# Optimization experiments

Measured on AMD Instinct MI355X. Metric: run time of the kernel, lower is better.

Reference implementation:

```python
import jax, jax.numpy as jnp
import numpy as np

B, QLEN, DIM = 16, 1, 4096
H, HKV, HD = 32, 8, 128  # n_heads, n_kv_heads, head_dim
PREFIX = 8192            # tokens already in the static KV cache


def setup_inputs() -> dict:
    key = jax.random.key(0)
    ks = jax.random.split(key, 7)
    s = 0.02
    return {
        "x": jax.random.normal(ks[0], (B, QLEN, DIM), jnp.float32),
        "cache_k": jax.random.normal(ks[1], (B, PREFIX, HKV, HD), jnp.float32),
        "cache_v": jax.random.normal(ks[2], (B, PREFIX, HKV, HD), jnp.float32),
        "wq": jax.random.normal(ks[3], (H * HD, DIM), jnp.float32) * s,
        "wk": jax.random.normal(ks[4], (HKV * HD, DIM), jnp.float32) * s,
        "wv": jax.random.normal(ks[5], (HKV * HD, DIM), jnp.float32) * s,
        "wo": jax.random.normal(ks[6], (DIM, H * HD), jnp.float32) * s,
    }


def reference(x, cache_k, cache_v, wq, wk, wv, wo):
    """Decode step of AttentionWithKVCache (static cache, GQA).

    Equivalent to: write new K/V at start_pos=PREFIX, attend q over
    cache[:, :PREFIX+QLEN], repeat_kv to expand kv heads, SDPA, out proj.
    """
    b, s, _ = x.shape
    q = (x @ wq.T).reshape(b, s, H, HD)        # [B,S,H,D]
    k_new = (x @ wk.T).reshape(b, s, HKV, HD)  # [B,S,Hkv,D]
    v_new = (x @ wv.T).reshape(b, s, HKV, HD)
    # cache write == concat of prefix with new tokens
    k = jnp.concatenate([cache_k, k_new], axis=1)  # [B,K,Hkv,D]
    v = jnp.concatenate([cache_v, v_new], axis=1)
    rep = H // HKV
    # repeat_kv: expand+reshape repeats each kv head `rep` times consecutively
    k = jnp.repeat(k, rep, axis=2)  # [B,K,H,D]
    v = jnp.repeat(v, rep, axis=2)
    scale = 1.0 / jnp.sqrt(jnp.asarray(HD, dtype=q.dtype))
    scores = jnp.einsum("bqhd,bkhd->bhqk", q, k) * scale
    attn = jax.nn.softmax(scores.astype(jnp.float32), axis=-1).astype(q.dtype)
    out = jnp.einsum("bhqk,bkhd->bqhd", attn, v).reshape(b, s, H * HD)
    return out @ wo.T  # [B,S,DIM]
```

## Files before the change

kernel.cpp:

```cpp
#include <hip/hip_runtime.h>
#include <hip/hip_bf16.h>
#include <cstdint>
#include <cstddef>

#define DIM 4096
#define NB 16
#define NH 32
#define NKV 8
#define HD 128
#define PREFIX 8192
#define KPB 256
#define KPW 64
#define NCH (PREFIX / KPB)
#define NPART NCH

#define WS_QKV 0
#define WS_ATT (WS_QKV + NB * 6144)
#define WS_ML  (WS_ATT + NB * DIM)
#define WS_OP  (WS_ML + NB * NCH * 32 * 2)

typedef float f4_t __attribute__((ext_vector_type(4)));
typedef float f2_t __attribute__((ext_vector_type(2)));
__device__ __forceinline__ float4 ntload4(const float* p) {
  f4_t v = __builtin_nontemporal_load((const f4_t*)p);
  return make_float4(v.x, v.y, v.z, v.w);
}
__device__ __forceinline__ float2 ntload2(const float* p) {
  f2_t v = __builtin_nontemporal_load((const f2_t*)p);
  return make_float2(v.x, v.y);
}

template <int NW>
__global__ __launch_bounds__(NW * 64) void gemv16(
    const float* __restrict__ W0, const float* __restrict__ W1,
    const float* __restrict__ W2, int b1, int b2,
    const float* __restrict__ X, float* __restrict__ Y,
    int y_stride, int scale_rows, float scale) {
  __shared__ float xs[NB][2048];
  const int tid = threadIdx.x;
  const int wave = tid >> 6, lane = tid & 63;
  const int row_base = blockIdx.x * (NW * 4) + wave * 4;

  const float* Wp;
  if (row_base < b1)       Wp = W0 + (size_t)row_base * DIM;
  else if (row_base < b2)  Wp = W1 + (size_t)(row_base - b1) * DIM;
  else                     Wp = W2 + (size_t)(row_base - b2) * DIM;

  float acc[4][NB];
#pragma unroll
  for (int r = 0; r < 4; ++r)
#pragma unroll
    for (int b = 0; b < NB; ++b) acc[r][b] = 0.0f;

  for (int k0 = 0; k0 < DIM; k0 += 2048) {
    __syncthreads();
#pragma unroll
    for (int i = 0; i < (8192 + NW * 64 - 1) / (NW * 64); ++i) {
      const int idx = tid + i * (NW * 64);
      if (idx < 8192) {
        const int b = idx >> 9, c = idx & 511;
        ((float4*)&xs[b][0])[c] =
            ((const float4*)(X + (size_t)b * DIM + k0))[c];
      }
    }
    __syncthreads();
#pragma unroll 4
    for (int ii = 0; ii < 8; ++ii) {
      const int d = ii * 256 + lane * 4;
      float4 w4[4];
#pragma unroll
      for (int r = 0; r < 4; ++r)
        w4[r] = ntload4(Wp + (size_t)r * DIM + k0 + d);
#pragma unroll
      for (int b = 0; b < NB; ++b) {
        float4 x4 = *(const float4*)&xs[b][d];
#pragma unroll
        for (int r = 0; r < 4; ++r)
          acc[r][b] += w4[r].x * x4.x + w4[r].y * x4.y +
                       w4[r].z * x4.z + w4[r].w * x4.w;
      }
    }
  }

#pragma unroll
  for (int r = 0; r < 4; ++r)
#pragma unroll
    for (int b = 0; b < NB; ++b) {
      float v = acc[r][b];
#pragma unroll
      for (int m = 1; m < 64; m <<= 1) v += __shfl_xor(v, m);
      acc[r][b] = v;
    }
  const int rsel = lane >> 4, bsel = lane & 15;
  float v = 0.0f;
#pragma unroll
  for (int r = 0; r < 4; ++r)
#pragma unroll
    for (int b = 0; b < NB; ++b)
      if (r == rsel && b == bsel) v = acc[r][b];
  const int row = row_base + rsel;
  if (row < scale_rows) v *= scale;
  Y[(size_t)bsel * y_stride + row] = v;
}

__global__ __launch_bounds__(256, 2) void attn_partial(
    const float* __restrict__ K, const float* __restrict__ V,
    const float* __restrict__ qkv, float* __restrict__ opart,
    float* __restrict__ mlpart) {
  __shared__ float lds[4 * 32 * 132];
  __shared__ float mw[4][32], lw[4][32];
  const int tid = threadIdx.x, wave = tid >> 6, lane = tid & 63;
  const int g = lane >> 3, soff = lane & 7;
  const int bid = blockIdx.x;
  const int c = bid & (NCH - 1), b = bid >> 5;

  float* scw = lds + wave * (KPW * 32);

  float4 qreg[4][4];
#pragma unroll
  for (int hh = 0; hh < 4; ++hh)
#pragma unroll
    for (int j = 0; j < 4; ++j)
      qreg[hh][j] = *(const float4*)(qkv + (size_t)b * 6144 +
                                     (g * 4 + hh) * HD + j * 32 + soff * 4);

  const size_t rowbase = ((size_t)b * PREFIX + c * KPB + wave * KPW) *
                         (NKV * HD);
  const float* kp = K + rowbase + g * HD + soff * 4;

  float mreg[4] = {-1e30f, -1e30f, -1e30f, -1e30f};
  for (int kb = 0; kb < KPW / 4; ++kb) {
    float4 k4[4][4];
#pragma unroll
    for (int kk = 0; kk < 4; ++kk)
#pragma unroll
      for (int j = 0; j < 4; ++j)
        k4[kk][j] =
            ntload4(kp + (size_t)(kb * 4 + kk) * (NKV * HD) + j * 32);
#pragma unroll
    for (int kk = 0; kk < 4; ++kk) {
      float p[4] = {0.f, 0.f, 0.f, 0.f};
#pragma unroll
      for (int j = 0; j < 4; ++j)
#pragma unroll
        for (int hh = 0; hh < 4; ++hh)
          p[hh] += qreg[hh][j].x * k4[kk][j].x + qreg[hh][j].y * k4[kk][j].y +
                   qreg[hh][j].z * k4[kk][j].z + qreg[hh][j].w * k4[kk][j].w;
#pragma unroll
      for (int mk = 1; mk < 8; mk <<= 1) {
        p[0] += __shfl_xor(p[0], mk);
        p[1] += __shfl_xor(p[1], mk);
        p[2] += __shfl_xor(p[2], mk);
        p[3] += __shfl_xor(p[3], mk);
      }
#pragma unroll
      for (int hh = 0; hh < 4; ++hh) mreg[hh] = fmaxf(mreg[hh], p[hh]);
      float wv = p[0];
      wv = (soff == 1) ? p[1] : wv;
      wv = (soff == 2) ? p[2] : wv;
      wv = (soff == 3) ? p[3] : wv;
      if (soff < 4) scw[(kb * 4 + kk) * 32 + g * 4 + soff] = wv;
    }
  }
  {
    float mv = mreg[0];
    mv = (soff == 1) ? mreg[1] : mv;
    mv = (soff == 2) ? mreg[2] : mv;
    mv = (soff == 3) ? mreg[3] : mv;
    if (soff < 4) mw[wave][g * 4 + soff] = mv;
  }
  asm volatile("s_waitcnt lgkmcnt(0)" ::: "memory");
  __builtin_amdgcn_sched_barrier(0);

  {
    const int gh = lane >> 1, half = lane & 1;
    const float m = mw[wave][gh];
    float lsum = 0.f;
#pragma unroll 8
    for (int i = 0; i < 32; ++i) {
      const int idx = (half * 32 + i) * 32 + gh;
      const float pe = __expf(scw[idx] - m);
      scw[idx] = pe;
      lsum += pe;
    }
    lsum += __shfl_xor(lsum, 1);
    if (half == 0) lw[wave][gh] = lsum;
  }
  asm volatile("s_waitcnt lgkmcnt(0)" ::: "memory");
  __builtin_amdgcn_sched_barrier(0);

  const float* vp = V + rowbase + g * HD + soff * 4;
  float4 acc[4][4];
#pragma unroll
  for (int hh = 0; hh < 4; ++hh)
#pragma unroll
    for (int j = 0; j < 4; ++j) acc[hh][j] = make_float4(0.f, 0.f, 0.f, 0.f);
  for (int kb = 0; kb < KPW / 4; ++kb) {
    float4 v4[4][4];
#pragma unroll
    for (int kk = 0; kk < 4; ++kk)
#pragma unroll
      for (int j = 0; j < 4; ++j)
        v4[kk][j] =
            ntload4(vp + (size_t)(kb * 4 + kk) * (NKV * HD) + j * 32);
#pragma unroll
    for (int kk = 0; kk < 4; ++kk) {
      float4 pr = *(const float4*)&scw[(kb * 4 + kk) * 32 + g * 4];
      const float prh[4] = {pr.x, pr.y, pr.z, pr.w};
#pragma unroll
      for (int hh = 0; hh < 4; ++hh)
#pragma unroll
        for (int j = 0; j < 4; ++j) {
          acc[hh][j].x += prh[hh] * v4[kk][j].x;
          acc[hh][j].y += prh[hh] * v4[kk][j].y;
          acc[hh][j].z += prh[hh] * v4[kk][j].z;
          acc[hh][j].w += prh[hh] * v4[kk][j].w;
        }
    }
  }

  __syncthreads();
  float* mb = lds + wave * (32 * 132);
#pragma unroll
  for (int hh = 0; hh < 4; ++hh)
#pragma unroll
    for (int j = 0; j < 4; ++j)
      *(float4*)(mb + (g * 4 + hh) * 132 + j * 32 + soff * 4) = acc[hh][j];
  __syncthreads();
  {
    const int gh = tid >> 3, sub = tid & 7;
    const float m0 = mw[0][gh], m1 = mw[1][gh], m2 = mw[2][gh], m3 = mw[3][gh];
    const float M = fmaxf(fmaxf(m0, m1), fmaxf(m2, m3));
    const float w0 = __expf(m0 - M), w1 = __expf(m1 - M);
    const float w2 = __expf(m2 - M), w3 = __expf(m3 - M);
    const float L = w0 * lw[0][gh] + w1 * lw[1][gh] +
                    w2 * lw[2][gh] + w3 * lw[3][gh];
    const size_t obase = ((size_t)bid * 32 + gh) * HD;
#pragma unroll
    for (int i = 0; i < 4; ++i) {
      const int d = sub * 16 + i * 4;
      float4 a0 = *(const float4*)(lds + 0 * 4224 + gh * 132 + d);
      float4 a1 = *(const float4*)(lds + 1 * 4224 + gh * 132 + d);
      float4 a2 = *(const float4*)(lds + 2 * 4224 + gh * 132 + d);
      float4 a3 = *(const float4*)(lds + 3 * 4224 + gh * 132 + d);
      float4 o;
      o.x = w0 * a0.x + w1 * a1.x + w2 * a2.x + w3 * a3.x;
      o.y = w0 * a0.y + w1 * a1.y + w2 * a2.y + w3 * a3.y;
      o.z = w0 * a0.z + w1 * a1.z + w2 * a2.z + w3 * a3.z;
      o.w = w0 * a0.w + w1 * a1.w + w2 * a2.w + w3 * a3.w;
      *(float4*)(opart + obase + d) = o;
    }
    if (sub == 0)
      *(float2*)(mlpart + ((size_t)bid * 32 + gh) * 2) = make_float2(M, L);
  }
}

__global__ __launch_bounds__(64) void combine(
    const float* __restrict__ opart, const float* __restrict__ mlpart,
    const float* __restrict__ qkv, float* __restrict__ aout) {
  const int bh = blockIdx.x;
  const int hg = bh & 31, b = bh >> 5;
  const int g = hg >> 2;
  const int lane = threadIdx.x;

  const float* qp = qkv + (size_t)b * 6144 + hg * HD;
  const float* kn = qkv + (size_t)b * 6144 + 4096 + g * HD;
  const float* vn = qkv + (size_t)b * 6144 + 5120 + g * HD;
  float2 q2 = *(const float2*)(qp + lane * 2);
  float2 k2 = *(const float2*)(kn + lane * 2);
  float sn = q2.x * k2.x + q2.y * k2.y;
#pragma unroll
  for (int mk = 1; mk < 64; mk <<= 1) sn += __shfl_xor(sn, mk);

  float M = sn;
#pragma unroll 8
  for (int c = 0; c < NPART; ++c)
    M = fmaxf(M, mlpart[((size_t)(b * NCH + c) * 32 + hg) * 2]);

  float L = 0, ax = 0, ay = 0;
#pragma unroll 8
  for (int c = 0; c < NPART; ++c) {
    const size_t pidx = (size_t)(b * NCH + c) * 32 + hg;
    const float mc = mlpart[pidx * 2 + 0];
    const float lc = mlpart[pidx * 2 + 1];
    const float w = __expf(mc - M);
    L += lc * w;
    float2 o2 = ntload2(opart + pidx * HD + lane * 2);
    ax += w * o2.x;
    ay += w * o2.y;
  }
  const float pn = __expf(sn - M);
  float2 v2 = *(const float2*)(vn + lane * 2);
  L += pn;
  ax += pn * v2.x;
  ay += pn * v2.y;

  const float inv = 1.0f / L;
  aout[(size_t)b * DIM + hg * HD + lane * 2 + 0] = ax * inv;
  aout[(size_t)b * DIM + hg * HD + lane * 2 + 1] = ay * inv;
}

extern "C" void kernel_launch(void* const* d_in, const int* in_sizes, int n_in,
                              void* d_out, int out_size, void* d_ws,
                              size_t ws_size, hipStream_t stream) {
  const float* x  = (const float*)d_in[0];
  const float* ck = (const float*)d_in[1];
  const float* cv = (const float*)d_in[2];
  const float* wq = (const float*)d_in[3];
  const float* wk = (const float*)d_in[4];
  const float* wv = (const float*)d_in[5];
  const float* wo = (const float*)d_in[6];
  float* out = (float*)d_out;
  float* ws = (float*)d_ws;

  float* qkv = ws + WS_QKV;
  float* att = ws + WS_ATT;
  float* ml  = ws + WS_ML;
  float* op  = ws + WS_OP;

  const float scale = 0.08838834764831845f;

  gemv16<6><<<256, 384, 0, stream>>>(wq, wk, wv, 4096, 5120, x, qkv, 6144,
                                     4096, scale);
  attn_partial<<<NB * NCH, 256, 0, stream>>>(ck, cv, qkv, op, ml);
  combine<<<NB * NH, 64, 0, stream>>>(op, ml, qkv, att);
  gemv16<4><<<256, 256, 0, stream>>>(wo, wo, wo, 4096, 4096, att, out, 4096,
                                     0, 1.0f);
}
```

Measured before the change: 244.6 us.

## Drop LDS staging in GEMV and spread rows over more blocks

```diff
diff --git a/kernel.cpp b/kernel.cpp
--- a/kernel.cpp
+++ b/kernel.cpp
@@ -30,60 +30,49 @@
   return make_float2(v.x, v.y);
 }
 
-template <int NW>
-__global__ __launch_bounds__(NW * 64) void gemv16(
+template <int ROWS>
+__global__ __launch_bounds__(256, 2) void gemv16(
     const float* __restrict__ W0, const float* __restrict__ W1,
     const float* __restrict__ W2, int b1, int b2,
     const float* __restrict__ X, float* __restrict__ Y,
     int y_stride, int scale_rows, float scale) {
-  __shared__ float xs[NB][2048];
   const int tid = threadIdx.x;
   const int wave = tid >> 6, lane = tid & 63;
-  const int row_base = blockIdx.x * (NW * 4) + wave * 4;
-
-  const float* Wp;
-  if (row_base < b1)       Wp = W0 + (size_t)row_base * DIM;
-  else if (row_base < b2)  Wp = W1 + (size_t)(row_base - b1) * DIM;
-  else                     Wp = W2 + (size_t)(row_base - b2) * DIM;
-
-  float acc[4][NB];
-#pragma unroll
-  for (int r = 0; r < 4; ++r)
+  const int row_base = blockIdx.x * (4 * ROWS) + wave * ROWS;
+
+  const float* Wr[ROWS];
+#pragma unroll
+  for (int r = 0; r < ROWS; ++r) {
+    const int row = row_base + r;
+    Wr[r] = (row < b1) ? W0 + (size_t)row * DIM
+          : (row < b2) ? W1 + (size_t)(row - b1) * DIM
+                       : W2 + (size_t)(row - b2) * DIM;
+  }
+
+  float acc[ROWS][NB];
+#pragma unroll
+  for (int r = 0; r < ROWS; ++r)
 #pragma unroll
     for (int b = 0; b < NB; ++b) acc[r][b] = 0.0f;
 
-  for (int k0 = 0; k0 < DIM; k0 += 2048) {
-    __syncthreads();
-#pragma unroll
-    for (int i = 0; i < (8192 + NW * 64 - 1) / (NW * 64); ++i) {
-      const int idx = tid + i * (NW * 64);
-      if (idx < 8192) {
-        const int b = idx >> 9, c = idx & 511;
-        ((float4*)&xs[b][0])[c] =
-            ((const float4*)(X + (size_t)b * DIM + k0))[c];
-      }
-    }
-    __syncthreads();
-#pragma unroll 4
-    for (int ii = 0; ii < 8; ++ii) {
-      const int d = ii * 256 + lane * 4;
-      float4 w4[4];
-#pragma unroll
-      for (int r = 0; r < 4; ++r)
-        w4[r] = ntload4(Wp + (size_t)r * DIM + k0 + d);
-#pragma unroll
-      for (int b = 0; b < NB; ++b) {
-        float4 x4 = *(const float4*)&xs[b][d];
-#pragma unroll
-        for (int r = 0; r < 4; ++r)
-          acc[r][b] += w4[r].x * x4.x + w4[r].y * x4.y +
-                       w4[r].z * x4.z + w4[r].w * x4.w;
-      }
-    }
-  }
-
-#pragma unroll
-  for (int r = 0; r < 4; ++r)
+#pragma unroll 2
+  for (int ii = 0; ii < 16; ++ii) {
+    const int d = ii * 256 + lane * 4;
+    float4 w4[ROWS];
+#pragma unroll
+    for (int r = 0; r < ROWS; ++r) w4[r] = ntload4(Wr[r] + d);
+#pragma unroll
+    for (int b = 0; b < NB; ++b) {
+      const float4 x4 = *(const float4*)(X + (size_t)b * DIM + d);
+#pragma unroll
+      for (int r = 0; r < ROWS; ++r)
+        acc[r][b] += w4[r].x * x4.x + w4[r].y * x4.y +
+                     w4[r].z * x4.z + w4[r].w * x4.w;
+    }
+  }
+
+#pragma unroll
+  for (int r = 0; r < ROWS; ++r)
 #pragma unroll
     for (int b = 0; b < NB; ++b) {
       float v = acc[r][b];
@@ -92,15 +81,17 @@
       acc[r][b] = v;
     }
   const int rsel = lane >> 4, bsel = lane & 15;
-  float v = 0.0f;
-#pragma unroll
-  for (int r = 0; r < 4; ++r)
-#pragma unroll
-    for (int b = 0; b < NB; ++b)
-      if (r == rsel && b == bsel) v = acc[r][b];
-  const int row = row_base + rsel;
-  if (row < scale_rows) v *= scale;
-  Y[(size_t)bsel * y_stride + row] = v;
+  if (rsel < ROWS) {
+    float v = 0.0f;
+#pragma unroll
+    for (int r = 0; r < ROWS; ++r)
+#pragma unroll
+      for (int b = 0; b < NB; ++b)
+        if (r == rsel && b == bsel) v = acc[r][b];
+    const int row = row_base + rsel;
+    if (row < scale_rows) v *= scale;
+    Y[(size_t)bsel * y_stride + row] = v;
+  }
 }
 
 __global__ __launch_bounds__(256, 2) void attn_partial(
@@ -320,10 +311,10 @@
 
   const float scale = 0.08838834764831845f;
 
-  gemv16<6><<<256, 384, 0, stream>>>(wq, wk, wv, 4096, 5120, x, qkv, 6144,
+  gemv16<3><<<512, 256, 0, stream>>>(wq, wk, wv, 4096, 5120, x, qkv, 6144,
                                      4096, scale);
   attn_partial<<<NB * NCH, 256, 0, stream>>>(ck, cv, qkv, op, ml);
   combine<<<NB * NH, 64, 0, stream>>>(op, ml, qkv, att);
-  gemv16<4><<<256, 256, 0, stream>>>(wo, wo, wo, 4096, 4096, att, out, 4096,
+  gemv16<2><<<512, 256, 0, stream>>>(wo, wo, wo, 4096, 4096, att, out, 4096,
                                      0, 1.0f);
 }
```

New measurement: 274.4 us. 1.12x slower.
